# Optimization experiments

Measured on AMD Instinct MI355X. Metric: run time of the kernel, lower is better.

Reference implementation:

```python
import jax, jax.numpy as jnp
import numpy as np

B, S, D, H, FF, V, L = 2, 2048, 1024, 16, 4096, 32000, 4
HD = D // H
SCALE = HD ** -0.5
STD = 0.02


def _ln(x, w, b, eps=1e-5):
    mu = jnp.mean(x, axis=-1, keepdims=True)
    var = jnp.mean(jnp.square(x - mu), axis=-1, keepdims=True)
    return (x - mu) * jax.lax.rsqrt(var + eps) * w + b


def setup_inputs() -> dict:
    key = jax.random.key(0)
    ks = iter(jax.random.split(key, 16))

    def w(k, shape):
        return jax.random.normal(k, shape, jnp.float32) * STD

    inp = {
        "tokens": jax.random.randint(next(ks), (B, S), 0, V, jnp.int32),
        "tok_emb": w(next(ks), (V, D)),
        "ln_e_w": jnp.ones((D,), jnp.float32),
        "ln_e_b": jnp.zeros((D,), jnp.float32),
        "ln1_w": jnp.ones((L, D), jnp.float32),
        "ln1_b": jnp.zeros((L, D), jnp.float32),
        "wq": w(next(ks), (L, D, D)),
        "bq": jnp.zeros((L, D), jnp.float32),
        "wk": w(next(ks), (L, D, D)),
        "bk": jnp.zeros((L, D), jnp.float32),
        "wv": w(next(ks), (L, D, D)),
        "bv": jnp.zeros((L, D), jnp.float32),
        "wo": w(next(ks), (L, D, D)),
        "bo": jnp.zeros((L, D), jnp.float32),
        "ln2_w": jnp.ones((L, D), jnp.float32),
        "ln2_b": jnp.zeros((L, D), jnp.float32),
        "w1": w(next(ks), (L, D, 2 * FF)),
        "b1": jnp.zeros((L, 2 * FF), jnp.float32),
        "w2": w(next(ks), (L, FF, D)),
        "b2": jnp.zeros((L, D), jnp.float32),
        "lnf_w": jnp.ones((D,), jnp.float32),
        "lnf_b": jnp.zeros((D,), jnp.float32),
        "w_out": w(next(ks), (D, V)),
        "b_out": jnp.zeros((V,), jnp.float32),
    }
    return inp


def reference(tokens, tok_emb, ln_e_w, ln_e_b, ln1_w, ln1_b, wq, bq, wk, bk,
              wv, bv, wo, bo, ln2_w, ln2_b, w1, b1, w2, b2, lnf_w, lnf_b,
              w_out, b_out):
    x = tok_emb[tokens]                      # [B,S,D]
    x = _ln(x, ln_e_w, ln_e_b)               # embedding LayerNorm (dropout off)
    for l in range(L):
        # pre-LN attention
        h = _ln(x, ln1_w[l], ln1_b[l])
        q = (h @ wq[l] + bq[l]).reshape(B, S, H, HD)
        k = (h @ wk[l] + bk[l]).reshape(B, S, H, HD)
        v = (h @ wv[l] + bv[l]).reshape(B, S, H, HD)
        scores = jnp.einsum('bqhd,bkhd->bhqk', q, k) * SCALE
        attn = jax.nn.softmax(scores, axis=-1)
        o = jnp.einsum('bhqk,bkhd->bqhd', attn, v).reshape(B, S, D)
        x = x + (o @ wo[l] + bo[l])
        # pre-LN gated (GeGLU) FFN
        h = _ln(x, ln2_w[l], ln2_b[l])
        gv = h @ w1[l] + b1[l]               # [B,S,2*FF]
        gate, val = gv[..., :FF], gv[..., FF:]
        ff = jax.nn.gelu(gate, approximate=False) * val
        x = x + (ff @ w2[l] + b2[l])
    x = _ln(x, lnf_w, lnf_b)
    return x @ w_out + b_out                 # logits [B,S,V]
```

## Files before the change

### kernel.cpp

```cpp
#include <hip/hip_runtime.h>

typedef __attribute__((ext_vector_type(8))) short s16x8;
typedef __attribute__((ext_vector_type(4))) short s16x4;
typedef __attribute__((ext_vector_type(4))) float f32x4;

__device__ __forceinline__ unsigned short f2bf(float f){
    union{float f;unsigned u;}v; v.f=f;
    unsigned u=v.u;
    unsigned r=(u+0x7fffu+((u>>16)&1u))>>16;
    return (unsigned short)r;
}
__device__ __forceinline__ float bf2f(unsigned short s){
    union{unsigned u;float f;}v; v.u=((unsigned)s)<<16; return v.f;
}
__device__ __forceinline__ unsigned pk2t(float a, float b){
    return (__float_as_uint(a)>>16) | (__float_as_uint(b) & 0xffff0000u);
}
__device__ __forceinline__ unsigned pk2r(float a, float b){
    return (unsigned)f2bf(a) | ((unsigned)f2bf(b)<<16);
}
__device__ __forceinline__ f32x4 fmax4(f32x4 a, f32x4 b){
    f32x4 r; r[0]=fmaxf(a[0],b[0]); r[1]=fmaxf(a[1],b[1]);
    r[2]=fmaxf(a[2],b[2]); r[3]=fmaxf(a[3],b[3]); return r;
}

__device__ __forceinline__ void gl16(const void* g, void* l){
    __builtin_amdgcn_global_load_lds(
        (const __attribute__((address_space(1))) void*)g,
        (__attribute__((address_space(3))) void*)l, 16, 0, 0);
}

#define ATT_SCALE 0.125f

__global__ __launch_bounds__(256) void flash_k(
    const unsigned short* __restrict__ qkv,
    const unsigned short* __restrict__ vt,
    unsigned short* __restrict__ o)
{
    __shared__ __align__(16) unsigned short Pl[4][2048];
    const int t=threadIdx.x, w=t>>6, lane=t&63;
    const int lr=lane&15, lg=lane>>4;
    const int zb=blockIdx.y>>4, zh=blockIdx.y&15;
    const long sr0 = (long)zb*2048 + blockIdx.x*128 + w*32;
    const unsigned short* qb    = qkv + sr0*3072 + zh*64;
    const unsigned short* kbase = qkv + ((long)zb*2048)*3072 + 1024 + zh*64;
    const unsigned short* vtb   = vt + (long)zb*2097152 + (long)zh*131072;

    s16x8 qf[2][2];
    #pragma unroll
    for(int qg=0;qg<2;qg++)
        #pragma unroll
        for(int kc=0;kc<2;kc++)
            qf[qg][kc] = *(const s16x8*)(qb + (qg*16+lr)*3072 + kc*32 + lg*8);

    float m0=-1e30f, m1=-1e30f, l0=0.f, l1=0.f;
    f32x4 oa[2][4];
    #pragma unroll
    for(int qg=0;qg<2;qg++)
        #pragma unroll
        for(int dt=0;dt<4;dt++) oa[qg][dt]=f32x4{0.f,0.f,0.f,0.f};

    char* Pw = (char*)&Pl[w][0];
    const int swz = (lr&7)<<4;

    for(int kv0=0; kv0<2048; kv0+=64){
        f32x4 s[2][4];
        #pragma unroll
        for(int kb=0;kb<4;kb++){
            const unsigned short* kr = kbase + (long)(kv0+kb*16+lr)*3072;
            s16x8 a0 = *(const s16x8*)(kr + lg*8);
            s16x8 a1 = *(const s16x8*)(kr + 32 + lg*8);
            #pragma unroll
            for(int qg=0;qg<2;qg++){
                f32x4 z4{0.f,0.f,0.f,0.f};
                z4 = __builtin_amdgcn_mfma_f32_16x16x32_bf16(a0, qf[qg][0], z4,0,0,0);
                s[qg][kb] = __builtin_amdgcn_mfma_f32_16x16x32_bf16(a1, qf[qg][1], z4,0,0,0);
            }
        }
        #pragma unroll
        for(int qg=0;qg<2;qg++){
            float& m = qg? m1:m0;
            float& l = qg? l1:l0;
            f32x4 mx4 = fmax4(fmax4(s[qg][0],s[qg][1]),fmax4(s[qg][2],s[qg][3]));
            float bm = fmaxf(fmaxf(mx4[0],mx4[1]),fmaxf(mx4[2],mx4[3]));
            bm = fmaxf(bm, __shfl_xor(bm,16));
            bm = fmaxf(bm, __shfl_xor(bm,32));
            const float mn = fmaxf(m, bm);
            const float sc = __expf((m-mn)*ATT_SCALE);
            m = mn;
            float rs=0.f;
            #pragma unroll
            for(int kb=0;kb<4;kb++){
                f32x4 p;
                #pragma unroll
                for(int r=0;r<4;r++){ p[r]=__expf((s[qg][kb][r]-mn)*ATT_SCALE); rs+=p[r]; }
                s[qg][kb]=p;
            }
            rs += __shfl_xor(rs,16);
            rs += __shfl_xor(rs,32);
            l = l*sc + rs;
            #pragma unroll
            for(int dt=0;dt<4;dt++) oa[qg][dt] = oa[qg][dt]*sc;
            #pragma unroll
            for(int kb=0;kb<4;kb++){
                uint2 pw;
                pw.x = pk2t(s[qg][kb][0], s[qg][kb][1]);
                pw.y = pk2t(s[qg][kb][2], s[qg][kb][3]);
                *(uint2*)(Pw + (qg*16+lr)*128 + ((kb*32+lg*8)^swz)) = pw;
            }
        }
        asm volatile("s_waitcnt lgkmcnt(0)" ::: "memory");
        s16x8 pb0[2], pb1[2];
        #pragma unroll
        for(int qg=0;qg<2;qg++){
            pb0[qg] = *(const s16x8*)(Pw + (qg*16+lr)*128 + ((     lg*16)^swz));
            pb1[qg] = *(const s16x8*)(Pw + (qg*16+lr)*128 + ((64 + lg*16)^swz));
        }
        #pragma unroll
        for(int dt=0;dt<4;dt++){
            const unsigned short* vr = vtb + (dt*16+lr)*2048 + kv0;
            s16x8 v0 = *(const s16x8*)(vr + lg*8);
            s16x8 v1 = *(const s16x8*)(vr + 32 + lg*8);
            #pragma unroll
            for(int qg=0;qg<2;qg++){
                oa[qg][dt] = __builtin_amdgcn_mfma_f32_16x16x32_bf16(v0, pb0[qg], oa[qg][dt],0,0,0);
                oa[qg][dt] = __builtin_amdgcn_mfma_f32_16x16x32_bf16(v1, pb1[qg], oa[qg][dt],0,0,0);
            }
        }
    }
    #pragma unroll
    for(int qg=0;qg<2;qg++){
        const float inv = 1.f/(qg? l1:l0);
        #pragma unroll
        for(int dt=0;dt<4;dt++){
            uint2 st;
            st.x = pk2r(oa[qg][dt][0]*inv, oa[qg][dt][1]*inv);
            st.y = pk2r(oa[qg][dt][2]*inv, oa[qg][dt][3]*inv);
            *(uint2*)(o + (sr0+qg*16+lr)*1024 + zh*64 + dt*16 + lg*4) = st;
        }
    }
}

template<bool OBF16,bool BIAS>
__global__ __launch_bounds__(512,2) void gemm8_k(
    const unsigned short* __restrict__ A,
    const unsigned short* __restrict__ B,
    const float* __restrict__ bias,
    void* __restrict__ Cp,
    int K,int lda,int ldb,int ldc)
{
    __shared__ __align__(16) char lds[131072];
    const int t=threadIdx.x, w=t>>6, lane=t&63;
    const int wr=w>>2, wc=w&3;
    const int lr=lane&15, lg=lane>>4;

    const int nwg = gridDim.x*gridDim.y;
    const int id  = blockIdx.y*gridDim.x + blockIdx.x;
    const int nid = (id&7)*(nwg>>3) + (id>>3);
    const long row0 = (long)(nid % gridDim.x)*256;
    const long col0 = (long)(nid / gridDim.x)*256;

    const int NT = K>>6;

    const int csw0 = (lg*16) ^ ((lr&7)<<4);
    const int aRow = (wr*64+lr)*128;
    const int bRow = (wc*32+lr)*128;

    const int sro = t>>3;
    const int sce = (((t&7) ^ ((t>>3)&7))<<3);

#define STAGE(gp, ld_, lb) do{ \
    const unsigned short* _g=(gp); char* _l=(lb); \
    gl16(_g + (long)sro*(ld_) + sce, _l + t*16); \
    gl16(_g + (long)(sro+64)*(ld_) + sce, _l + 8192 + t*16); }while(0)

#define LDA8(m,kk) (*(const s16x8*)(Ab_ + aRow + ((m)&3)*2048 + ((m)>>2)*16384 + ((kk)? (csw0^64):csw0)))
#define LDB8(n,kk) (*(const s16x8*)(Bb_ + bRow + ((n)&1)*2048 + ((n)>>1)*16384 + ((kk)? (csw0^64):csw0)))

    f32x4 acc[8][4];
    #pragma unroll
    for(int m=0;m<8;m++)
        #pragma unroll
        for(int n=0;n<4;n++) acc[m][n]=f32x4{0.f,0.f,0.f,0.f};

    STAGE(A + row0*lda,        lda, lds);
    STAGE(B + col0*ldb,        ldb, lds+65536);
    STAGE(A + (row0+128)*lda,  lda, lds+16384);
    STAGE(B + (col0+128)*ldb,  ldb, lds+65536+16384);
    STAGE(A + row0*lda + 64,   lda, lds+32768);
    STAGE(B + col0*ldb + 64,   ldb, lds+65536+32768);
    asm volatile("s_waitcnt vmcnt(4)" ::: "memory");
    __builtin_amdgcn_s_barrier();

    for(int tt=0; tt<NT; ++tt){
        char* Ab_ = lds + ((tt&1)<<15);
        char* Bb_ = lds + 65536 + ((tt&1)<<15);
        char* An  = lds + (((tt+1)&1)<<15);
        char* Bn  = lds + 65536 + (((tt+1)&1)<<15);
        const int k1=(tt+1)<<6, k2=(tt+2)<<6;
        s16x8 a[4][2], b01[2][2], b23[2][2];

        #pragma unroll
        for(int m=0;m<4;m++){ a[m][0]=LDA8(m,0); a[m][1]=LDA8(m,1); }
        #pragma unroll
        for(int n=0;n<2;n++){ b01[n][0]=LDB8(n,0); b01[n][1]=LDB8(n,1); }
        if(tt+1<NT) STAGE(A + (row0+128)*lda + k1, lda, An+16384);
        __builtin_amdgcn_s_barrier();
        __builtin_amdgcn_s_setprio(1);
        #pragma unroll
        for(int kk=0;kk<2;kk++)
            #pragma unroll
            for(int m=0;m<4;m++)
                #pragma unroll
                for(int n=0;n<2;n++)
                    acc[m][n]=__builtin_amdgcn_mfma_f32_16x16x32_bf16(a[m][kk],b01[n][kk],acc[m][n],0,0,0);
        __builtin_amdgcn_s_setprio(0);
        __builtin_amdgcn_s_barrier();

        #pragma unroll
        for(int n=0;n<2;n++){ b23[n][0]=LDB8(n+2,0); b23[n][1]=LDB8(n+2,1); }
        if(tt+1<NT) STAGE(B + (col0+128)*ldb + k1, ldb, Bn+16384);
        __builtin_amdgcn_s_barrier();
        __builtin_amdgcn_s_setprio(1);
        #pragma unroll
        for(int kk=0;kk<2;kk++)
            #pragma unroll
            for(int m=0;m<4;m++)
                #pragma unroll
                for(int n=0;n<2;n++)
                    acc[m][n+2]=__builtin_amdgcn_mfma_f32_16x16x32_bf16(a[m][kk],b23[n][kk],acc[m][n+2],0,0,0);
        __builtin_amdgcn_s_setprio(0);
        __builtin_amdgcn_s_barrier();

        #pragma unroll
        for(int m=0;m<4;m++){ a[m][0]=LDA8(m+4,0); a[m][1]=LDA8(m+4,1); }
        if(tt+2<NT) STAGE(A + row0*lda + k2, lda, Ab_);
        __builtin_amdgcn_s_barrier();
        __builtin_amdgcn_s_setprio(1);
        #pragma unroll
        for(int kk=0;kk<2;kk++)
            #pragma unroll
            for(int m=0;m<4;m++)
                #pragma unroll
                for(int n=0;n<2;n++)
                    acc[m+4][n]=__builtin_amdgcn_mfma_f32_16x16x32_bf16(a[m][kk],b01[n][kk],acc[m+4][n],0,0,0);
        __builtin_amdgcn_s_setprio(0);
        __builtin_amdgcn_s_barrier();

        if(tt+2<NT) STAGE(B + col0*ldb + k2, ldb, Bb_);
        __builtin_amdgcn_s_barrier();
        __builtin_amdgcn_s_setprio(1);
        #pragma unroll
        for(int kk=0;kk<2;kk++)
            #pragma unroll
            for(int m=0;m<4;m++)
                #pragma unroll
                for(int n=0;n<2;n++)
                    acc[m+4][n+2]=__builtin_amdgcn_mfma_f32_16x16x32_bf16(a[m][kk],b23[n][kk],acc[m+4][n+2],0,0,0);
        __builtin_amdgcn_s_setprio(0);
        if(tt+2<NT) asm volatile("s_waitcnt vmcnt(4)" ::: "memory");
        else        asm volatile("s_waitcnt vmcnt(0)" ::: "memory");
        __builtin_amdgcn_s_barrier();
    }

    #pragma unroll
    for(int m=0;m<8;m++){
        #pragma unroll
        for(int n=0;n<4;n++){
            #pragma unroll
            for(int rr=0;rr<4;rr++){
                const long grow = row0 + wr*64 + (m&3)*16 + (m>>2)*128 + lg*4 + rr;
                const long gcol = col0 + wc*32 + (n&1)*16 + (n>>1)*128 + lr;
                float vv = acc[m][n][rr];
                if constexpr(BIAS) vv += bias[gcol];
                if constexpr(OBF16) ((unsigned short*)Cp)[grow*(long)ldc+gcol]=f2bf(vv);
                else                ((float*)Cp)[grow*(long)ldc+gcol]=vv;
            }
        }
    }
#undef STAGE
#undef LDA8
#undef LDB8
}

__global__ __launch_bounds__(256) void gelu8_k(const unsigned short* __restrict__ gv,
                                               unsigned short* __restrict__ ff)
{
    const long total8 = (long)4096*4096/8;
    for(long i8=(long)blockIdx.x*256+threadIdx.x; i8<total8; i8+=(long)gridDim.x*256){
        const long idx=i8*8;
        const long r=idx>>12; const int c=(int)(idx&4095);
        s16x8 g8=*(const s16x8*)(gv + r*8192 + c);
        s16x8 v8=*(const s16x8*)(gv + r*8192 + 4096 + c);
        s16x8 o8;
        #pragma unroll
        for(int i=0;i<8;i++){
            float gg=bf2f((unsigned short)g8[i]);
            float vl=bf2f((unsigned short)v8[i]);
            float ge=0.5f*gg*(1.f+erff(gg*0.70710678118654752f));
            o8[i]=(short)f2bf(ge*vl);
        }
        *(s16x8*)(ff+idx)=o8;
    }
}

__global__ __launch_bounds__(256) void cat3_k(const float* __restrict__ a,
    const float* __restrict__ b, const float* __restrict__ c,
    float* __restrict__ out)
{
    const int i = blockIdx.x*256+threadIdx.x;
    const int l = i/3072, cc = i%3072;
    float v = (cc<1024)? a[l*1024+cc] : (cc<2048)? b[l*1024+cc-1024] : c[l*1024+cc-2048];
    out[i]=v;
}

template<int BM,int BN,int WN,bool BIAS,bool RES,bool OBF16,bool SCL,bool SWAP,bool GEGLU>
__global__ __launch_bounds__(256) void gemm_bt(
    const unsigned short* __restrict__ A,
    const unsigned short* __restrict__ B,
    const unsigned short* __restrict__ B2,
    const float* __restrict__ bias,
    const float* __restrict__ res,
    void* __restrict__ Cp,
    int K,int lda,int ldb,int ldc,
    long aSb,long aSh,long bSb,long bSh,long cSb,long cSh,int zH)
{
    constexpr int BK=64;
    constexpr int WM=4/WN, WTM=BM/WM, WTN=BN/WN;
    constexpr int FM=WTM/16, FN=WTN/16;
    constexpr int CA=BM/8, CB=BN/8;
    __shared__ __align__(16) unsigned short As[BM*BK];
    __shared__ __align__(16) unsigned short Bs[BN*BK*(GEGLU?2:1)];

    const int t=threadIdx.x, w=t>>6, lane=t&63;
    const int wr=w/WN, wc=w%WN;
    const int lr=lane&15, lg=lane>>4;
    const int z=blockIdx.z, zb=z/zH, zh=z%zH;
    const long row0 = SWAP ? (long)blockIdx.x*BM : (long)blockIdx.y*BM;
    const long col0 = SWAP ? (long)blockIdx.y*BN : (long)blockIdx.x*BN;

    const unsigned short* Ab = A + zb*aSb + zh*aSh;
    const unsigned short* Bb = B + zb*bSb + zh*bSh;

    const int lr8 = lane>>3;
    const int lc8 = (lane&7)<<3;

    f32x4 acc[FM][FN];
    f32x4 acc2[GEGLU?FM:1][GEGLU?FN:1];
    #pragma unroll
    for(int i=0;i<FM;i++)
        #pragma unroll
        for(int j=0;j<FN;j++){
            acc[i][j]=f32x4{0.f,0.f,0.f,0.f};
            if constexpr(GEGLU) acc2[i][j]=f32x4{0.f,0.f,0.f,0.f};
        }

    const int NT=K/BK;
    for(int kt=0;kt<NT;kt++){
        const int kb=kt*BK;
        #pragma unroll
        for(int cc=0;cc<CA/4;cc++){
            const int c=cc*4+w;
            gl16(Ab + (row0 + c*8 + lr8)*(long)lda + kb + lc8, (char*)As + c*1024);
        }
        #pragma unroll
        for(int cc=0;cc<CB/4;cc++){
            const int c=cc*4+w;
            gl16(Bb + (col0 + c*8 + lr8)*(long)ldb + kb + lc8, (char*)Bs + c*1024);
        }
        if constexpr(GEGLU){
            #pragma unroll
            for(int cc=0;cc<CB/4;cc++){
                const int c=cc*4+w;
                gl16(B2 + (col0 + c*8 + lr8)*(long)ldb + kb + lc8,
                     (char*)Bs + (CB + c)*1024);
            }
        }
        __syncthreads();
        const unsigned short* Arp = As + (wr*WTM+lr)*BK + lg*8;
        const unsigned short* Brp = Bs + (wc*WTN+lr)*BK + lg*8;
        #pragma unroll
        for(int kk=0;kk<2;kk++){
            s16x8 af[FM], bfv[FN], bf2[GEGLU?FN:1];
            #pragma unroll
            for(int i=0;i<FM;i++) af[i] = *(const s16x8*)(Arp + i*16*BK + kk*32);
            #pragma unroll
            for(int j=0;j<FN;j++) bfv[j]= *(const s16x8*)(Brp + j*16*BK + kk*32);
            if constexpr(GEGLU){
                #pragma unroll
                for(int j=0;j<FN;j++) bf2[j]=*(const s16x8*)(Brp + BN*BK + j*16*BK + kk*32);
            }
            #pragma unroll
            for(int i=0;i<FM;i++)
                #pragma unroll
                for(int j=0;j<FN;j++){
                    acc[i][j]=__builtin_amdgcn_mfma_f32_16x16x32_bf16(af[i],bfv[j],acc[i][j],0,0,0);
                    if constexpr(GEGLU)
                        acc2[i][j]=__builtin_amdgcn_mfma_f32_16x16x32_bf16(af[i],bf2[j],acc2[i][j],0,0,0);
                }
        }
        __syncthreads();
    }
    #pragma unroll
    for(int i=0;i<FM;i++){
        #pragma unroll
        for(int j=0;j<FN;j++){
            #pragma unroll
            for(int r=0;r<4;r++){
                const long grow = row0 + wr*WTM + i*16 + lg*4 + r;
                const long gcol = col0 + wc*WTN + j*16 + lr;
                if constexpr(GEGLU){
                    float g  = acc[i][j][r]  + bias[gcol];
                    float vl = acc2[i][j][r] + bias[gcol+4096];
                    float ge = 0.5f*g*(1.f+erff(g*0.70710678118654752f));
                    ((unsigned short*)Cp)[grow*ldc+gcol] = f2bf(ge*vl);
                } else {
                    float vv=acc[i][j][r];
                    if constexpr(SCL)  vv*=ATT_SCALE;
                    if constexpr(BIAS) vv+=bias[gcol];
                    if constexpr(RES)  vv+=res[grow*ldc+gcol];
                    const long cidx = zb*cSb + zh*cSh + grow*ldc + gcol;
                    if constexpr(OBF16) ((unsigned short*)Cp)[cidx]=f2bf(vv);
                    else                ((float*)Cp)[cidx]=vv;
                }
            }
        }
    }
}

template<bool IN32>
__global__ __launch_bounds__(256) void tr_k(const void* __restrict__ in,
    unsigned short* __restrict__ out, int ldin, int ldout,
    long inZb, long inZh, long outZb, long outZh, int zH)
{
    __shared__ unsigned short tl[64][68];
    const int t=threadIdx.x;
    const int z=blockIdx.z, zb=z/zH, zh=z%zH;
    const long ib=(long)blockIdx.x*64*ldin + (long)blockIdx.y*64 + zb*inZb + zh*inZh;
    const long ob=(long)blockIdx.y*64*ldout + (long)blockIdx.x*64 + zb*outZb + zh*outZh;
    const int r0=t>>4, c0=(t&15)*4;
    #pragma unroll
    for(int p=0;p<4;p++){
        const int rr=r0+p*16;
        if constexpr(IN32){
            f32x4 v=*(const f32x4*)((const float*)in + ib + (long)rr*ldin + c0);
            #pragma unroll
            for(int i=0;i<4;i++) tl[c0+i][rr]=f2bf(v[i]);
        } else {
            s16x4 v=*(const s16x4*)((const unsigned short*)in + ib + (long)rr*ldin + c0);
            #pragma unroll
            for(int i=0;i<4;i++) tl[c0+i][rr]=(unsigned short)v[i];
        }
    }
    __syncthreads();
    #pragma unroll
    for(int p=0;p<4;p++){
        const int rr=r0+p*16;
        s16x4 o4;
        #pragma unroll
        for(int i=0;i<4;i++) o4[i]=(short)tl[rr][c0+i];
        *(s16x4*)(out + ob + (long)rr*ldout + c0)=o4;
    }
}

template<bool GATHER, bool OBF16>
__global__ __launch_bounds__(256) void ln_k(const float* __restrict__ in,
    const float* __restrict__ w, const float* __restrict__ b,
    void* __restrict__ out, const int* __restrict__ tok)
{
    const int row = blockIdx.x, t = threadIdx.x;
    const float* src;
    if constexpr (GATHER) src = in + (long)tok[row]*1024;
    else                  src = in + (long)row*1024;
    const int c = t*4;
    f32x4 xv = *(const f32x4*)(src + c);
    float s  = xv[0]+xv[1]+xv[2]+xv[3];
    float qq = xv[0]*xv[0]+xv[1]*xv[1]+xv[2]*xv[2]+xv[3]*xv[3];
    #pragma unroll
    for(int m=32;m;m>>=1){ s += __shfl_xor(s,m); qq += __shfl_xor(qq,m); }
    __shared__ float rs_[4], rq_[4];
    if((t&63)==0){ rs_[t>>6]=s; rq_[t>>6]=qq; }
    __syncthreads();
    s  = rs_[0]+rs_[1]+rs_[2]+rs_[3];
    qq = rq_[0]+rq_[1]+rq_[2]+rq_[3];
    const float mu = s*(1.f/1024.f);
    const float rstd = rsqrtf(qq*(1.f/1024.f)-mu*mu + 1e-5f);
    f32x4 wv = *(const f32x4*)(w+c), bv = *(const f32x4*)(b+c);
    if constexpr (OBF16){
        s16x4 ov;
        #pragma unroll
        for(int i=0;i<4;i++) ov[i]=(short)f2bf((xv[i]-mu)*rstd*wv[i]+bv[i]);
        *(s16x4*)((unsigned short*)out + (long)row*1024 + c) = ov;
    } else {
        f32x4 ov;
        #pragma unroll
        for(int i=0;i<4;i++) ov[i]=(xv[i]-mu)*rstd*wv[i]+bv[i];
        *(f32x4*)((float*)out + (long)row*1024 + c) = ov;
    }
}

template<int BM,int BN,int WN,bool BIAS>
__global__ __launch_bounds__(256) void gemm_k(
    const unsigned short* __restrict__ A,
    const float* __restrict__ Bp,
    const float* __restrict__ bias,
    float* __restrict__ Cp,
    int K,int lda,int ldb,int ldc)
{
    constexpr int BK=64, PAD=24, LDS_=BK+PAD;
    constexpr int WM = 4/WN;
    constexpr int WTM = BM/WM, WTN = BN/WN;
    constexpr int FM = WTM/16, FN = WTN/16;
    __shared__ unsigned short As[BM*LDS_];
    __shared__ unsigned short Bs[BN*LDS_];

    const int t = threadIdx.x;
    const int w = t>>6, lane = t&63;
    const int wr = w / WN, wc = w % WN;
    const int lr = lane & 15, lg = lane >> 4;

    const long row0 = (long)blockIdx.y*BM;
    const long col0 = (long)blockIdx.x*BN;

    f32x4 acc[FM][FN];
    #pragma unroll
    for(int i=0;i<FM;i++)
        #pragma unroll
        for(int j=0;j<FN;j++) acc[i][j] = f32x4{0.f,0.f,0.f,0.f};

    const int NT = K/BK;
    for(int kt=0; kt<NT; ++kt){
        const int kb = kt*BK;
        {
            constexpr int PASS = BM*BK/(256*4);
            #pragma unroll
            for(int p=0;p<PASS;p++){
                int idx = (p*256+t)*4;
                int r = idx/BK, c = idx%BK;
                *(s16x4*)&As[r*LDS_+c] = *(const s16x4*)(A + (row0+r)*lda + kb + c);
            }
        }
        {
            constexpr int TPB = 256/BN;
            constexpr int KC  = BK/TPB;
            const int n = t % BN, k0 = (t/BN)*KC;
            #pragma unroll
            for(int j0=0;j0<KC;j0+=8){
                s16x8 pk;
                #pragma unroll
                for(int i=0;i<8;i++){
                    const long gk = (long)kb + k0 + j0 + i;
                    pk[i] = (short)f2bf(Bp[gk*ldb + col0 + n]);
                }
                *(s16x8*)&Bs[n*LDS_ + k0 + j0] = pk;
            }
        }
        __syncthreads();
        const unsigned short* Ar = &As[(wr*WTM + lr)*LDS_ + lg*8];
        const unsigned short* Br = &Bs[(wc*WTN + lr)*LDS_ + lg*8];
        #pragma unroll
        for(int kk=0;kk<BK/32;kk++){
            s16x8 af[FM], bfv[FN];
            #pragma unroll
            for(int i=0;i<FM;i++) af[i]  = *(const s16x8*)(Ar + i*16*LDS_ + kk*32);
            #pragma unroll
            for(int j=0;j<FN;j++) bfv[j] = *(const s16x8*)(Br + j*16*LDS_ + kk*32);
            #pragma unroll
            for(int i=0;i<FM;i++)
                #pragma unroll
                for(int j=0;j<FN;j++)
                    acc[i][j] = __builtin_amdgcn_mfma_f32_16x16x32_bf16(af[i],bfv[j],acc[i][j],0,0,0);
        }
        __syncthreads();
    }
    #pragma unroll
    for(int i=0;i<FM;i++){
        #pragma unroll
        for(int j=0;j<FN;j++){
            #pragma unroll
            for(int r=0;r<4;r++){
                long grow = row0 + wr*WTM + i*16 + lg*4 + r;
                long gcol = col0 + wc*WTN + j*16 + lr;
                float vv = acc[i][j][r];
                if constexpr (BIAS) vv += bias[gcol];
                Cp[grow*ldc + gcol] = vv;
            }
        }
    }
}

extern "C" void kernel_launch(void* const* d_in, const int* in_sizes, int n_in,
                              void* d_out, int out_size, void* d_ws, size_t ws_size,
                              hipStream_t stream)
{
    const int*   tokens  = (const int*)  d_in[0];
    const float* tok_emb = (const float*)d_in[1];
    const float* ln_e_w  = (const float*)d_in[2];
    const float* ln_e_b  = (const float*)d_in[3];
    const float* ln1_w   = (const float*)d_in[4];
    const float* ln1_b   = (const float*)d_in[5];
    const float* wq      = (const float*)d_in[6];
    const float* bq      = (const float*)d_in[7];
    const float* wk      = (const float*)d_in[8];
    const float* bk      = (const float*)d_in[9];
    const float* wv      = (const float*)d_in[10];
    const float* bv      = (const float*)d_in[11];
    const float* wo      = (const float*)d_in[12];
    const float* bo      = (const float*)d_in[13];
    const float* ln2_w   = (const float*)d_in[14];
    const float* ln2_b   = (const float*)d_in[15];
    const float* w1      = (const float*)d_in[16];
    const float* b1      = (const float*)d_in[17];
    const float* w2      = (const float*)d_in[18];
    const float* b2      = (const float*)d_in[19];
    const float* lnf_w   = (const float*)d_in[20];
    const float* lnf_b   = (const float*)d_in[21];
    const float* w_out   = (const float*)d_in[22];
    const float* b_out   = (const float*)d_in[23];

    const int D=1024;
    const long DD  = (long)D*D;
    const long WQKV_L = 3145728L;

    unsigned short* gv8 = (unsigned short*)d_out;

    unsigned short *wqkvT,*woT,*w1T,*w2T,*woutT=nullptr;
    float *x,*bqkv;
    unsigned short *h,*qkv,*vt,*o,*ff;
    bool fastTier;
    if (ws_size >= 301989888ull){
        char* p=(char*)d_ws;
        wqkvT=(unsigned short*)(p);
        woT  =(unsigned short*)(p+25165824);
        w1T  =(unsigned short*)(p+33554432);
        w2T  =(unsigned short*)(p+100663296);
        woutT=(unsigned short*)(p+134217728);
        x    =(float*)(p+201326592);
        h    =(unsigned short*)(p+218103808);
        qkv  =(unsigned short*)(p+226492416);
        vt   =(unsigned short*)(p+251658240);
        o    =(unsigned short*)(p+260046848);
        ff   =(unsigned short*)(p+268435456);
        bqkv =(float*)((char*)d_out + 134217728);
        fastTier=true;
    } else {
        char* p=(char*)d_out;
        qkv  =(unsigned short*)(p);
        bqkv =(float*)(p+25165824);
        wqkvT=(unsigned short*)(p+268435456);
        woT  =(unsigned short*)(p+293601280);
        w1T  =(unsigned short*)(p+301989888);
        w2T  =(unsigned short*)(p+369098752);
        x    =(float*)(p+402653184);
        vt   =(unsigned short*)(p+444596224);
        o    =(unsigned short*)(p+452984832);
        ff   =(unsigned short*)(p+461373440);
        h    =(unsigned short*)d_ws;
        fastTier=false;
    }

    const dim3 blk(256,1,1), blk8(512,1,1);

    tr_k<true><<<dim3(16,16,4), blk,0,stream>>>(wq, wqkvT,           1024,1024, DD,0, WQKV_L,0, 1);
    tr_k<true><<<dim3(16,16,4), blk,0,stream>>>(wk, wqkvT+1048576,   1024,1024, DD,0, WQKV_L,0, 1);
    tr_k<true><<<dim3(16,16,4), blk,0,stream>>>(wv, wqkvT+2097152,   1024,1024, DD,0, WQKV_L,0, 1);
    tr_k<true><<<dim3(16,16,4), blk,0,stream>>>(wo, woT, 1024,1024, DD,0, DD,0, 1);
    tr_k<true><<<dim3(16,128,4),blk,0,stream>>>(w1, w1T, 8192,1024, 8388608L,0, 8388608L,0, 1);
    tr_k<true><<<dim3(64,16,4), blk,0,stream>>>(w2, w2T, 1024,4096, 4194304L,0, 4194304L,0, 1);
    if (fastTier)
        tr_k<true><<<dim3(16,500,1),blk,0,stream>>>(w_out, woutT, 32000,1024, 0,0, 0,0, 1);
    cat3_k<<<48,blk,0,stream>>>(bq, bk, bv, bqkv);

    ln_k<true,false><<<4096,blk,0,stream>>>(tok_emb, ln_e_w, ln_e_b, x, tokens);

    const dim3 g_d(8,32,1);

    for(int l=0;l<4;l++){
        ln_k<false,true><<<4096,blk,0,stream>>>(x, ln1_w+l*D, ln1_b+l*D, h, nullptr);
        gemm8_k<true,true><<<dim3(16,12,1),blk8,0,stream>>>(
            h, wqkvT+l*WQKV_L, bqkv+l*3072, qkv, 1024, 1024,1024,3072);
        tr_k<false><<<dim3(32,1,32),blk,0,stream>>>(qkv+2048, vt, 3072,2048,
            2048L*3072,64, 2097152L,131072L, 16);
        flash_k<<<dim3(16,32,1),blk,0,stream>>>(qkv, vt, o);
        gemm_bt<128,128,2,true,true,false,false,false,false><<<g_d,blk,0,stream>>>(
            o, woT+l*DD, nullptr, bo+l*D, x, x, 1024, 1024,1024,1024, 0,0,0,0,0,0, 1);
        ln_k<false,true><<<4096,blk,0,stream>>>(x, ln2_w+l*D, ln2_b+l*D, h, nullptr);
        if (fastTier){
            gemm8_k<true,true><<<dim3(16,32,1),blk8,0,stream>>>(
                h, w1T+l*8388608L, b1+(long)l*8192, gv8, 1024, 1024,1024,8192);
            gelu8_k<<<2048,blk,0,stream>>>(gv8, ff);
        } else {
            gemm_bt<128,64,1,true,false,true,false,false,true><<<dim3(64,32,1),blk,0,stream>>>(
                h, w1T+l*8388608L, w1T+l*8388608L+4194304L, b1+(long)l*8192, nullptr, ff,
                1024, 1024,1024,4096, 0,0,0,0,0,0, 1);
        }
        gemm_bt<128,128,2,true,true,false,false,false,false><<<g_d,blk,0,stream>>>(
            ff, w2T+l*4194304L, nullptr, b2+l*D, x, x, 4096, 4096,4096,1024, 0,0,0,0,0,0, 1);
    }

    ln_k<false,true><<<4096,blk,0,stream>>>(x, lnf_w, lnf_b, h, nullptr);

    if (fastTier){
        gemm8_k<false,true><<<dim3(16,125,1),blk8,0,stream>>>(
            h, woutT, b_out, (float*)d_out, 1024, 1024,1024,32000);
    } else {
        gemm_k<128,128,2,true><<<dim3(250,32,1),blk,0,stream>>>(
            h, w_out, b_out, (float*)d_out, 1024, 1024,32000,32000);
    }
}
```

Measured before the change: 2.176 ms.

## Fuse GeGLU into FFN1 GEMM epilogue, stage fp32 stores via LDS, tune flash priorities

```diff
diff --git a/kernel.cpp b/kernel.cpp
--- a/kernel.cpp
+++ b/kernel.cpp
@@ -65,6 +65,7 @@
 
     for(int kv0=0; kv0<2048; kv0+=64){
         f32x4 s[2][4];
+        __builtin_amdgcn_s_setprio(1);
         #pragma unroll
         for(int kb=0;kb<4;kb++){
             const unsigned short* kr = kbase + (long)(kv0+kb*16+lr)*3072;
@@ -76,6 +77,14 @@
                 z4 = __builtin_amdgcn_mfma_f32_16x16x32_bf16(a0, qf[qg][0], z4,0,0,0);
                 s[qg][kb] = __builtin_amdgcn_mfma_f32_16x16x32_bf16(a1, qf[qg][1], z4,0,0,0);
             }
+        }
+        __builtin_amdgcn_s_setprio(0);
+        s16x8 vreg[4][2];
+        #pragma unroll
+        for(int dt=0;dt<4;dt++){
+            const unsigned short* vr = vtb + (dt*16+lr)*2048 + kv0;
+            vreg[dt][0] = *(const s16x8*)(vr + lg*8);
+            vreg[dt][1] = *(const s16x8*)(vr + 32 + lg*8);
         }
         #pragma unroll
         for(int qg=0;qg<2;qg++){
@@ -116,17 +125,16 @@
             pb0[qg] = *(const s16x8*)(Pw + (qg*16+lr)*128 + ((     lg*16)^swz));
             pb1[qg] = *(const s16x8*)(Pw + (qg*16+lr)*128 + ((64 + lg*16)^swz));
         }
+        __builtin_amdgcn_s_setprio(1);
         #pragma unroll
         for(int dt=0;dt<4;dt++){
-            const unsigned short* vr = vtb + (dt*16+lr)*2048 + kv0;
-            s16x8 v0 = *(const s16x8*)(vr + lg*8);
-            s16x8 v1 = *(const s16x8*)(vr + 32 + lg*8);
             #pragma unroll
             for(int qg=0;qg<2;qg++){
-                oa[qg][dt] = __builtin_amdgcn_mfma_f32_16x16x32_bf16(v0, pb0[qg], oa[qg][dt],0,0,0);
-                oa[qg][dt] = __builtin_amdgcn_mfma_f32_16x16x32_bf16(v1, pb1[qg], oa[qg][dt],0,0,0);
-            }
-        }
+                oa[qg][dt] = __builtin_amdgcn_mfma_f32_16x16x32_bf16(vreg[dt][0], pb0[qg], oa[qg][dt],0,0,0);
+                oa[qg][dt] = __builtin_amdgcn_mfma_f32_16x16x32_bf16(vreg[dt][1], pb1[qg], oa[qg][dt],0,0,0);
+            }
+        }
+        __builtin_amdgcn_s_setprio(0);
     }
     #pragma unroll
     for(int qg=0;qg<2;qg++){
@@ -141,7 +149,7 @@
     }
 }
 
-template<bool OBF16,bool BIAS>
+template<bool OBF16,bool BIAS,bool GEGLU>
 __global__ __launch_bounds__(512,2) void gemm8_k(
     const unsigned short* __restrict__ A,
     const unsigned short* __restrict__ B,
@@ -263,45 +271,71 @@
         __builtin_amdgcn_s_barrier();
     }
 
-    #pragma unroll
-    for(int m=0;m<8;m++){
-        #pragma unroll
-        for(int n=0;n<4;n++){
-            #pragma unroll
-            for(int rr=0;rr<4;rr++){
-                const long grow = row0 + wr*64 + (m&3)*16 + (m>>2)*128 + lg*4 + rr;
-                const long gcol = col0 + wc*32 + (n&1)*16 + (n>>1)*128 + lr;
-                float vv = acc[m][n][rr];
-                if constexpr(BIAS) vv += bias[gcol];
-                if constexpr(OBF16) ((unsigned short*)Cp)[grow*(long)ldc+gcol]=f2bf(vv);
-                else                ((float*)Cp)[grow*(long)ldc+gcol]=vv;
+    if constexpr(GEGLU){
+        const long hc0 = col0>>1;
+        #pragma unroll
+        for(int m=0;m<8;m++){
+            #pragma unroll
+            for(int n=0;n<2;n++){
+                #pragma unroll
+                for(int rr=0;rr<4;rr++){
+                    const long grow = row0 + wr*64 + (m&3)*16 + (m>>2)*128 + lg*4 + rr;
+                    const long g    = hc0 + wc*32 + n*16 + lr;
+                    float gg = acc[m][n][rr]   + bias[g];
+                    float vl = acc[m][n+2][rr] + bias[4096+g];
+                    float ge = 0.5f*gg*(1.f+erff(gg*0.70710678118654752f));
+                    ((unsigned short*)Cp)[grow*(long)ldc + g] = f2bf(ge*vl);
+                }
+            }
+        }
+    } else if constexpr(!OBF16){
+        float* L = (float*)lds;
+        const int lc4 = (t&63)*4;
+        f32x4 bv{0.f,0.f,0.f,0.f};
+        if constexpr(BIAS) bv = *(const f32x4*)(bias + col0 + lc4);
+        #pragma unroll
+        for(int ch=0; ch<2; ch++){
+            __builtin_amdgcn_s_barrier();
+            #pragma unroll
+            for(int mm=0;mm<4;mm++){
+                #pragma unroll
+                for(int n=0;n<4;n++){
+                    #pragma unroll
+                    for(int rr=0;rr<4;rr++){
+                        const int lrow = wr*64 + mm*16 + lg*4 + rr;
+                        const int lcol = wc*32 + (n&1)*16 + (n>>1)*128 + lr;
+                        L[lrow*256 + lcol] = acc[ch*4+mm][n][rr];
+                    }
+                }
+            }
+            __builtin_amdgcn_s_barrier();
+            #pragma unroll
+            for(int p=0;p<16;p++){
+                const int lrow = p*8 + (t>>6);
+                f32x4 v4 = *(const f32x4*)(L + lrow*256 + lc4);
+                if constexpr(BIAS){ v4[0]+=bv[0]; v4[1]+=bv[1]; v4[2]+=bv[2]; v4[3]+=bv[3]; }
+                *(f32x4*)((float*)Cp + (row0 + ch*128 + lrow)*(long)ldc + col0 + lc4) = v4;
+            }
+        }
+    } else {
+        #pragma unroll
+        for(int m=0;m<8;m++){
+            #pragma unroll
+            for(int n=0;n<4;n++){
+                #pragma unroll
+                for(int rr=0;rr<4;rr++){
+                    const long grow = row0 + wr*64 + (m&3)*16 + (m>>2)*128 + lg*4 + rr;
+                    const long gcol = col0 + wc*32 + (n&1)*16 + (n>>1)*128 + lr;
+                    float vv = acc[m][n][rr];
+                    if constexpr(BIAS) vv += bias[gcol];
+                    ((unsigned short*)Cp)[grow*(long)ldc+gcol]=f2bf(vv);
+                }
             }
         }
     }
 #undef STAGE
 #undef LDA8
 #undef LDB8
-}
-
-__global__ __launch_bounds__(256) void gelu8_k(const unsigned short* __restrict__ gv,
-                                               unsigned short* __restrict__ ff)
-{
-    const long total8 = (long)4096*4096/8;
-    for(long i8=(long)blockIdx.x*256+threadIdx.x; i8<total8; i8+=(long)gridDim.x*256){
-        const long idx=i8*8;
-        const long r=idx>>12; const int c=(int)(idx&4095);
-        s16x8 g8=*(const s16x8*)(gv + r*8192 + c);
-        s16x8 v8=*(const s16x8*)(gv + r*8192 + 4096 + c);
-        s16x8 o8;
-        #pragma unroll
-        for(int i=0;i<8;i++){
-            float gg=bf2f((unsigned short)g8[i]);
-            float vl=bf2f((unsigned short)v8[i]);
-            float ge=0.5f*gg*(1.f+erff(gg*0.70710678118654752f));
-            o8[i]=(short)f2bf(ge*vl);
-        }
-        *(s16x8*)(ff+idx)=o8;
-    }
 }
 
 __global__ __launch_bounds__(256) void cat3_k(const float* __restrict__ a,
@@ -428,7 +462,7 @@
     }
 }
 
-template<bool IN32>
+template<bool IN32, bool REMAP>
 __global__ __launch_bounds__(256) void tr_k(const void* __restrict__ in,
     unsigned short* __restrict__ out, int ldin, int ldout,
     long inZb, long inZh, long outZb, long outZh, int zH)
@@ -437,7 +471,12 @@
     const int t=threadIdx.x;
     const int z=blockIdx.z, zb=z/zH, zh=z%zH;
     const long ib=(long)blockIdx.x*64*ldin + (long)blockIdx.y*64 + zb*inZb + zh*inZh;
-    const long ob=(long)blockIdx.y*64*ldout + (long)blockIdx.x*64 + zb*outZb + zh*outZh;
+    long orow = (long)blockIdx.y*64;
+    if constexpr(REMAP){
+        orow = (orow < 4096) ? ((orow>>7)*256 + (orow&127))
+                             : (((orow-4096)>>7)*256 + 128 + ((orow-4096)&127));
+    }
+    const long ob=orow*ldout + (long)blockIdx.x*64 + zb*outZb + zh*outZh;
     const int r0=t>>4, c0=(t&15)*4;
     #pragma unroll
     for(int p=0;p<4;p++){
@@ -621,8 +660,6 @@
     const int D=1024;
     const long DD  = (long)D*D;
     const long WQKV_L = 3145728L;
-
-    unsigned short* gv8 = (unsigned short*)d_out;
 
     unsigned short *wqkvT,*woT,*w1T,*w2T,*woutT=nullptr;
     float *x,*bqkv;
@@ -661,14 +698,17 @@
 
     const dim3 blk(256,1,1), blk8(512,1,1);
 
-    tr_k<true><<<dim3(16,16,4), blk,0,stream>>>(wq, wqkvT,           1024,1024, DD,0, WQKV_L,0, 1);
-    tr_k<true><<<dim3(16,16,4), blk,0,stream>>>(wk, wqkvT+1048576,   1024,1024, DD,0, WQKV_L,0, 1);
-    tr_k<true><<<dim3(16,16,4), blk,0,stream>>>(wv, wqkvT+2097152,   1024,1024, DD,0, WQKV_L,0, 1);
-    tr_k<true><<<dim3(16,16,4), blk,0,stream>>>(wo, woT, 1024,1024, DD,0, DD,0, 1);
-    tr_k<true><<<dim3(16,128,4),blk,0,stream>>>(w1, w1T, 8192,1024, 8388608L,0, 8388608L,0, 1);
-    tr_k<true><<<dim3(64,16,4), blk,0,stream>>>(w2, w2T, 1024,4096, 4194304L,0, 4194304L,0, 1);
-    if (fastTier)
-        tr_k<true><<<dim3(16,500,1),blk,0,stream>>>(w_out, woutT, 32000,1024, 0,0, 0,0, 1);
+    tr_k<true,false><<<dim3(16,16,4), blk,0,stream>>>(wq, wqkvT,         1024,1024, DD,0, WQKV_L,0, 1);
+    tr_k<true,false><<<dim3(16,16,4), blk,0,stream>>>(wk, wqkvT+1048576, 1024,1024, DD,0, WQKV_L,0, 1);
+    tr_k<true,false><<<dim3(16,16,4), blk,0,stream>>>(wv, wqkvT+2097152, 1024,1024, DD,0, WQKV_L,0, 1);
+    tr_k<true,false><<<dim3(16,16,4), blk,0,stream>>>(wo, woT, 1024,1024, DD,0, DD,0, 1);
+    if (fastTier){
+        tr_k<true,true><<<dim3(16,128,4),blk,0,stream>>>(w1, w1T, 8192,1024, 8388608L,0, 8388608L,0, 1);
+        tr_k<true,false><<<dim3(16,500,1),blk,0,stream>>>(w_out, woutT, 32000,1024, 0,0, 0,0, 1);
+    } else {
+        tr_k<true,false><<<dim3(16,128,4),blk,0,stream>>>(w1, w1T, 8192,1024, 8388608L,0, 8388608L,0, 1);
+    }
+    tr_k<true,false><<<dim3(64,16,4), blk,0,stream>>>(w2, w2T, 1024,4096, 4194304L,0, 4194304L,0, 1);
     cat3_k<<<48,blk,0,stream>>>(bq, bk, bv, bqkv);
 
     ln_k<true,false><<<4096,blk,0,stream>>>(tok_emb, ln_e_w, ln_e_b, x, tokens);
@@ -677,18 +717,17 @@
 
     for(int l=0;l<4;l++){
         ln_k<false,true><<<4096,blk,0,stream>>>(x, ln1_w+l*D, ln1_b+l*D, h, nullptr);
-        gemm8_k<true,true><<<dim3(16,12,1),blk8,0,stream>>>(
+        gemm8_k<true,true,false><<<dim3(16,12,1),blk8,0,stream>>>(
             h, wqkvT+l*WQKV_L, bqkv+l*3072, qkv, 1024, 1024,1024,3072);
-        tr_k<false><<<dim3(32,1,32),blk,0,stream>>>(qkv+2048, vt, 3072,2048,
+        tr_k<false,false><<<dim3(32,1,32),blk,0,stream>>>(qkv+2048, vt, 3072,2048,
             2048L*3072,64, 2097152L,131072L, 16);
         flash_k<<<dim3(16,32,1),blk,0,stream>>>(qkv, vt, o);
         gemm_bt<128,128,2,true,true,false,false,false,false><<<g_d,blk,0,stream>>>(
             o, woT+l*DD, nullptr, bo+l*D, x, x, 1024, 1024,1024,1024, 0,0,0,0,0,0, 1);
         ln_k<false,true><<<4096,blk,0,stream>>>(x, ln2_w+l*D, ln2_b+l*D, h, nullptr);
         if (fastTier){
-            gemm8_k<true,true><<<dim3(16,32,1),blk8,0,stream>>>(
-                h, w1T+l*8388608L, b1+(long)l*8192, gv8, 1024, 1024,1024,8192);
-            gelu8_k<<<2048,blk,0,stream>>>(gv8, ff);
+            gemm8_k<true,true,true><<<dim3(16,32,1),blk8,0,stream>>>(
+                h, w1T+l*8388608L, b1+(long)l*8192, ff, 1024, 1024,1024,4096);
         } else {
             gemm_bt<128,64,1,true,false,true,false,false,true><<<dim3(64,32,1),blk,0,stream>>>(
                 h, w1T+l*8388608L, w1T+l*8388608L+4194304L, b1+(long)l*8192, nullptr, ff,
@@ -701,7 +740,7 @@
     ln_k<false,true><<<4096,blk,0,stream>>>(x, lnf_w, lnf_b, h, nullptr);
 
     if (fastTier){
-        gemm8_k<false,true><<<dim3(16,125,1),blk8,0,stream>>>(
+        gemm8_k<false,true,false><<<dim3(16,125,1),blk8,0,stream>>>(
             h, woutT, b_out, (float*)d_out, 1024, 1024,1024,32000);
     } else {
         gemm_k<128,128,2,true><<<dim3(250,32,1),blk,0,stream>>>(
```

Result: faster. 1.998 ms (-8.1%).
